# Performance work log

Hardware: AMD Instinct MI355X
Metric: run time of the kernel (lower is better)

The kernel has to match this reference:

```python
import jax, jax.numpy as jnp
import numpy as np

B, N, L, C, H = 8, 300, 4096, 256, 8
DH = C // H  # 32; doubled to 64 after concat with pos/sine embeddings


def _linear_params(key, fan_in, fan_out):
    kw, kb = jax.random.split(key)
    bound = 1.0 / np.sqrt(fan_in)
    W = jax.random.uniform(kw, (fan_out, fan_in), jnp.float32, -bound, bound)
    b = jax.random.uniform(kb, (fan_out,), jnp.float32, -bound, bound)
    return W, b


def setup_inputs() -> dict:
    key = jax.random.key(0)
    ks = jax.random.split(key, 13)
    inp = {
        "query": jax.random.normal(ks[0], (B, N, C), jnp.float32),
        "key": jax.random.normal(ks[1], (B, L, C), jnp.float32),
        "value": jax.random.normal(ks[2], (B, L, C), jnp.float32),
        "query_pos": jax.random.normal(ks[3], (B, N, C), jnp.float32),
        "key_pos": jax.random.normal(ks[4], (B, L, C), jnp.float32),
        "query_sine_embed": jax.random.normal(ks[5], (B, N, C), jnp.float32),
    }
    names = ["qc", "qp", "qs", "kc", "kp", "v", "o"]
    for i, nm in enumerate(names):
        W, b = _linear_params(ks[6 + i], C, C)
        inp[f"W{nm}"] = W
        inp[f"b{nm}"] = b
    return inp


def reference(query, key, value, query_pos, key_pos, query_sine_embed,
              Wqc, bqc, Wqp, bqp, Wqs, bqs, Wkc, bkc, Wkp, bkp, Wv, bv, Wo, bo):
    lin = lambda x, W, b: jnp.einsum("bnc,dc->bnd", x, W) + b
    qc = lin(query, Wqc, bqc)                  # (B, N, C)
    kc = lin(key, Wkc, bkc)                    # (B, L, C)
    v = lin(value, Wv, bv)                     # (B, L, C)
    kp = lin(key_pos, Wkp, bkp)                # (B, L, C)
    qp = lin(query_pos, Wqp, bqp)              # is_first=True branch
    q = qc + qp
    k = kc + kp
    qs = lin(query_sine_embed, Wqs, bqs)
    # split heads and concat content with positional/sine embedding -> head dim 2*DH
    q = jnp.concatenate([q.reshape(B, N, H, DH), qs.reshape(B, N, H, DH)], axis=3)   # (B,N,H,2DH)
    k = jnp.concatenate([k.reshape(B, L, H, DH), kp.reshape(B, L, H, DH)], axis=3)   # (B,L,H,2DH)
    vh = v.reshape(B, L, H, DH)
    scale = (2 * DH) ** -0.5
    attn = jnp.einsum("bnhd,blhd->bhnl", q * scale, k)      # (B,H,N,L)
    attn = jax.nn.softmax(attn, axis=-1)
    out = jnp.einsum("bhnl,blhd->bnhd", attn, vh).reshape(B, N, C)
    out = jnp.einsum("bnc,dc->bnd", out, Wo) + bo
    return query + out  # identity = query
```

## Files before the change

### kernel.cpp

```cpp
#include <hip/hip_runtime.h>
#include <hip/hip_bf16.h>

using bf8_t = __attribute__((ext_vector_type(8))) short;
using bf4_t = __attribute__((ext_vector_type(4))) short;
using u16x4 = __attribute__((ext_vector_type(4))) unsigned short;
using f32x4 = __attribute__((ext_vector_type(4))) float;

constexpr int B_   = 8;
constexpr int N_   = 300;
constexpr int L_   = 4096;
constexpr int C_   = 256;
constexpr int H_   = 8;
constexpr int NPAD = 320;
constexpr int QT_  = 5;
constexpr int SPL_ = 4;
constexpr int TPS_ = 16;
constexpr float SCALE = 0.18033688011112042f;

__device__ __forceinline__ unsigned short f2b(float f) {
  unsigned u = __float_as_uint(f);
  u += 0x7FFFu + ((u >> 16) & 1u);
  return (unsigned short)(u >> 16);
}

__device__ __forceinline__ void stage_cvt16(unsigned short* dst, const float* src) {
#pragma unroll
  for (int half = 0; half < 2; ++half) {
    f32x4 x0 = *(const f32x4*)(src + half * 8);
    f32x4 x1 = *(const f32x4*)(src + half * 8 + 4);
    bf8_t v;
#pragma unroll
    for (int j = 0; j < 4; ++j) { v[j] = (short)f2b(x0[j]); v[4 + j] = (short)f2b(x1[j]); }
    *(bf8_t*)(dst + half * 8) = v;
  }
}

__device__ __forceinline__ void gload_lds16(const void* g, void* l) {
  __builtin_amdgcn_global_load_lds(
      (const __attribute__((address_space(1))) unsigned int*)g,
      (__attribute__((address_space(3))) unsigned int*)l, 16, 0, 0);
}

__device__ __forceinline__ unsigned cvt_pk_bf16(float lo, float hi) {
  unsigned r;
  asm("v_cvt_pk_bf16_f32 %0, %1, %2" : "=v"(r) : "v"(lo), "v"(hi));
  return r;
}

__global__ __launch_bounds__(256) void wcvt_k(
    const float* __restrict__ W0, const float* __restrict__ W1, const float* __restrict__ W2,
    unsigned short* __restrict__ Wq)
{
  const float* W[3] = {W0, W1, W2};
  const int kt = blockIdx.x, i = blockIdx.y;
  const int d = threadIdx.x;
  const float* src = W[i] + (size_t)d * C_ + kt * 64;
  unsigned short* dst = Wq + ((size_t)(i * 4 + kt) * 256 + d) * 64;
#pragma unroll
  for (int g = 0; g < 8; ++g) {
    f32x4 a = *(const f32x4*)(src + g * 8);
    f32x4 b = *(const f32x4*)(src + g * 8 + 4);
    bf8_t v;
#pragma unroll
    for (int j = 0; j < 4; ++j) { v[j] = (short)f2b(a[j]); v[4 + j] = (short)f2b(b[j]); }
    *(bf8_t*)(dst + (g ^ (d & 7)) * 8) = v;
  }
}

__global__ __launch_bounds__(256) void wcvt2_k(
    const float* __restrict__ W0, const float* __restrict__ W1, const float* __restrict__ W2,
    unsigned short* __restrict__ Wk)
{
  const float* W[3] = {W0, W1, W2};
  const int kt = blockIdx.x, i = blockIdx.y;
  const int d = threadIdx.x;
  const float* src = W[i] + (size_t)d * C_ + kt * 32;
  unsigned short* dst = Wk + ((size_t)(i * 8 + kt) * 256 + d) * 32;
#pragma unroll
  for (int g = 0; g < 4; ++g) {
    f32x4 a = *(const f32x4*)(src + g * 8);
    f32x4 b = *(const f32x4*)(src + g * 8 + 4);
    bf8_t v;
#pragma unroll
    for (int j = 0; j < 4; ++j) { v[j] = (short)f2b(a[j]); v[4 + j] = (short)f2b(b[j]); }
    *(bf8_t*)(dst + (g ^ (d & 3)) * 8) = v;
  }
}

__global__ __launch_bounds__(256, 4) void kvproj_k(
    const float* __restrict__ xp, const float* __restrict__ xk, const float* __restrict__ xv,
    const unsigned short* __restrict__ Wk,
    const float* __restrict__ bkp, const float* __restrict__ bkc, const float* __restrict__ bv,
    unsigned short* __restrict__ Kc, unsigned short* __restrict__ Kp, unsigned short* __restrict__ Vt)
{
  __shared__ __align__(16) unsigned short LB[20480];
  const int tid = threadIdx.x, lane = tid & 63, wv = tid >> 6;
  const int fr = lane & 15, fg = lane >> 4;
  const int i = blockIdx.y;
  const int row0 = blockIdx.x * 64;
  const int b = row0 >> 12, ll0 = row0 & (L_ - 1);
  const float* X    = (i == 0) ? xp  : (i == 1) ? xk  : xv;
  const float* bias = (i == 0) ? bkp : (i == 1) ? bkc : bv;

  const int ar = tid >> 2, ac = tid & 3;
  const int agx = (ac ^ (ar & 3)) * 8;

  f32x4 acc[4][4] = {};

  const unsigned short* Wi = Wk + (size_t)i * 8 * 8192;

  auto stageB = [&](int step, int buf) {
    const char* src = (const char*)(Wi + step * 8192);
    char* dst = (char*)(LB + 4096 + buf * 8192);
#pragma unroll
    for (int c = 0; c < 4; ++c) {
      const int off = c * 4096 + tid * 16;
      gload_lds16(src + off, dst + off);
    }
  };
  auto stageA_load = [&](int step, f32x4* arg) {
    const float* s = X + (size_t)(row0 + ar) * C_ + step * 32 + ac * 8;
    arg[0] = *(const f32x4*)s;
    arg[1] = *(const f32x4*)(s + 4);
  };
  auto stageA_write = [&](int buf, const f32x4* arg) {
    bf8_t v;
#pragma unroll
    for (int j = 0; j < 4; ++j) { v[j] = (short)f2b(arg[0][j]); v[4 + j] = (short)f2b(arg[1][j]); }
    *(bf8_t*)(LB + buf * 2048 + ar * 32 + agx) = v;
  };

  {
    f32x4 a0[2];
    stageA_load(0, a0);
    stageB(0, 0);
    stageA_write(0, a0);
  }
  __syncthreads();

  int cur = 0;
  const int gx = (fg ^ (fr & 3)) * 8;
  for (int step = 0; step < 8; ++step) {
    const int nxt = cur ^ 1;
    f32x4 arn[2];
    if (step < 7) {
      stageA_load(step + 1, arn);
      stageB(step + 1, nxt);
    }
    const unsigned short* Ab = LB + cur * 2048;
    const unsigned short* Bb = LB + 4096 + cur * 8192;
    bf8_t xf[4];
#pragma unroll
    for (int mt = 0; mt < 4; ++mt)
      xf[mt] = *(const bf8_t*)(Ab + (mt * 16 + fr) * 32 + gx);
#pragma unroll
    for (int nt = 0; nt < 4; ++nt) {
      bf8_t wf = *(const bf8_t*)(Bb + (wv * 64 + nt * 16 + fr) * 32 + gx);
#pragma unroll
      for (int mt = 0; mt < 4; ++mt)
        acc[nt][mt] = __builtin_amdgcn_mfma_f32_16x16x32_bf16(wf, xf[mt], acc[nt][mt], 0, 0, 0);
    }
    if (step < 7) stageA_write(nxt, arn);
    __syncthreads();
    cur = nxt;
  }

  if (i < 2) {
    unsigned short* outp = (i == 0) ? Kp : Kc;
#pragma unroll
    for (int nt = 0; nt < 4; ++nt) {
      const int d0 = wv * 64 + nt * 16 + fg * 4;
      const f32x4 bb = *(const f32x4*)(bias + d0);
      const int h = d0 >> 5, dh = d0 & 31;
#pragma unroll
      for (int mt = 0; mt < 4; ++mt) {
        const int l = ll0 + mt * 16 + fr;
        u16x4 v;
#pragma unroll
        for (int r = 0; r < 4; ++r) v[r] = f2b(acc[nt][mt][r] + bb[r]);
        *(u16x4*)(outp + ((size_t)(b * H_ + h) * L_ + l) * 32 + dh) = v;
      }
    }
  } else {
    unsigned short* T = LB;
#pragma unroll
    for (int nt = 0; nt < 4; ++nt) {
      const int d0 = wv * 64 + nt * 16 + fg * 4;
      const f32x4 bb = *(const f32x4*)(bias + d0);
#pragma unroll
      for (int mt = 0; mt < 4; ++mt)
#pragma unroll
        for (int r = 0; r < 4; ++r)
          T[(d0 + r) * 68 + mt * 16 + fr] = f2b(acc[nt][mt][r] + bb[r]);
    }
    __syncthreads();
    const int d = tid;
    unsigned short* dst = Vt + ((size_t)(b * H_ + (d >> 5)) * 32 + (d & 31)) * L_ + ll0;
#pragma unroll
    for (int j = 0; j < 16; ++j)
      *(u16x4*)(dst + j * 4) = *(const u16x4*)(T + d * 68 + j * 4);
  }
}

__global__ __launch_bounds__(256, 2) void qproj_k(
    const float* __restrict__ xp, const float* __restrict__ xq, const float* __restrict__ xs,
    const unsigned short* __restrict__ Wq,
    const float* __restrict__ bqp, const float* __restrict__ bqc, const float* __restrict__ bqs,
    unsigned short* __restrict__ Qcat)
{
  __shared__ __align__(16) unsigned short Al[2][64 * 64];
  __shared__ __align__(16) unsigned short Bl[2][256 * 64];
  const int tid = threadIdx.x, lane = tid & 63, wv = tid >> 6;
  const int fr = lane & 15, fg = lane >> 4;
  const int b = blockIdx.x / 5, n0 = (blockIdx.x % 5) * 64;
  const float* Ax[3] = {xp, xq, xs};

  const int sr = tid >> 2, sc = (tid & 3) * 16;
  const int ag = sc >> 3;
  const bool arow_ok = (n0 + sr) < N_;

  f32x4 acc[16] = {};

  auto stageB = [&](int step, int buf) {
    const char* bsrc = (const char*)Wq + (size_t)step * 32768;
    char* bdst = (char*)&Bl[buf][0];
#pragma unroll
    for (int c = 0; c < 8; ++c) {
      const int off = c * 4096 + wv * 1024 + lane * 16;
      gload_lds16(bsrc + off, bdst + off);
    }
  };
  auto stageA_load = [&](int step, f32x4* ar) {
    const int i = step >> 2, kt = step & 3;
    if (arow_ok) {
      const float* src = Ax[i] + ((size_t)b * N_ + n0 + sr) * C_ + kt * 64 + sc;
#pragma unroll
      for (int j = 0; j < 4; ++j) ar[j] = *(const f32x4*)(src + j * 4);
    } else {
#pragma unroll
      for (int j = 0; j < 4; ++j) ar[j] = (f32x4){0.f, 0.f, 0.f, 0.f};
    }
  };
  auto stageA_write = [&](int buf, const f32x4* ar) {
    unsigned short* base = &Al[buf][sr * 64];
    bf8_t v0, v1;
#pragma unroll
    for (int j = 0; j < 4; ++j) {
      v0[j] = (short)f2b(ar[0][j]); v0[4 + j] = (short)f2b(ar[1][j]);
      v1[j] = (short)f2b(ar[2][j]); v1[4 + j] = (short)f2b(ar[3][j]);
    }
    *(bf8_t*)(base + ((ag ^ (sr & 7)) * 8))       = v0;
    *(bf8_t*)(base + (((ag | 1) ^ (sr & 7)) * 8)) = v1;
  };

  {
    f32x4 a0[4];
    stageA_load(0, a0);
    stageB(0, 0);
    stageA_write(0, a0);
  }
  __syncthreads();

  int cur = 0;
  const int xrow = wv * 16 + fr;
  const int n_out = n0 + wv * 16 + fr;
  const bool ok = n_out < N_;
  for (int step = 0; step < 12; ++step) {
    const int nxt = cur ^ 1;
    f32x4 arn[4];
    if (step < 11) {
      stageA_load(step + 1, arn);
      stageB(step + 1, nxt);
    }
    const unsigned short* Ab = &Al[cur][0];
    const unsigned short* Bb = &Bl[cur][0];
#pragma unroll
    for (int kh = 0; kh < 2; ++kh) {
      const int gxx = (4 * kh + fg) ^ (fr & 7);
      bf8_t xf = *(const bf8_t*)(Ab + xrow * 64 + gxx * 8);
#pragma unroll
      for (int nt = 0; nt < 16; ++nt) {
        bf8_t wf = *(const bf8_t*)(Bb + (nt * 16 + fr) * 64 + gxx * 8);
        acc[nt] = __builtin_amdgcn_mfma_f32_16x16x32_bf16(wf, xf, acc[nt], 0, 0, 0);
      }
    }
    if (step == 7 || step == 11) {
      const int off = (step == 7) ? 0 : 32;
#pragma unroll
      for (int nt = 0; nt < 16; ++nt) {
        const int d0 = nt * 16 + fg * 4;
        f32x4 bb = *(const f32x4*)(bqp + d0) + *(const f32x4*)(bqc + d0);
        if (step == 11) bb += *(const f32x4*)(bqs + d0);
        u16x4 v;
#pragma unroll
        for (int r = 0; r < 4; ++r) v[r] = ok ? f2b((acc[nt][r] + bb[r]) * SCALE) : (unsigned short)0;
        *(u16x4*)(Qcat + ((size_t)(b * H_ + (d0 >> 5)) * NPAD + n_out) * 64 + off + (d0 & 31)) = v;
      }
    }
    if (step < 11) stageA_write(nxt, arn);
    __syncthreads();
    cur = nxt;
  }
}

__global__ __launch_bounds__(256, 5) void attn_k(
    const unsigned short* __restrict__ Qcat, const unsigned short* __restrict__ Kc,
    const unsigned short* __restrict__ Kp, const unsigned short* __restrict__ Vt,
    float* __restrict__ PO, float* __restrict__ PM, float* __restrict__ PLs)
{
  __shared__ __align__(16) unsigned short Kcl[2][64 * 32];
  __shared__ __align__(16) unsigned short Kpl[2][64 * 32];
  __shared__ __align__(16) unsigned short Vp[2][32][72];
  const int x = blockIdx.x;
  const int qt = x >> 8;
  const int rem = x & 255;
  const int s = rem & (SPL_ - 1);
  const int h = (rem >> 2) & (H_ - 1);
  const int b = rem >> 5;
  const int n0 = qt * 64;
  const int tid = threadIdx.x, lane = tid & 63, wv = tid >> 6;
  const int fr = lane & 15, fg = lane >> 4;

  const unsigned short* Qb = Qcat + ((size_t)b * H_ + h) * NPAD * 64;
  bf8_t qf[2];
  {
    const int qrow = n0 + wv * 16 + fr;
    qf[0] = *(const bf8_t*)&Qb[(size_t)qrow * 64 + 8 * fg];
    qf[1] = *(const bf8_t*)&Qb[(size_t)qrow * 64 + 32 + 8 * fg];
  }
  float m_r = -1e30f, l_r = 0.f;
  f32x4 o[2] = {};

  const unsigned short* KcB = Kc + ((size_t)b * H_ + h) * L_ * 32;
  const unsigned short* KpB = Kp + ((size_t)b * H_ + h) * L_ * 32;
  const unsigned short* VB  = Vt + ((size_t)b * H_ + h) * 32 * (size_t)L_;

  const int koff = tid * 16;
  const int vd = tid >> 3, vc = (tid & 7) * 8;

  auto stageK = [&](int t, int buf) {
    gload_lds16((const char*)KcB + (size_t)t * 4096 + koff, (char*)&Kcl[buf][0] + koff);
    gload_lds16((const char*)KpB + (size_t)t * 4096 + koff, (char*)&Kpl[buf][0] + koff);
  };

  const int t0 = s * TPS_, t1 = t0 + TPS_;

  stageK(t0, 0);
  bf8_t vreg = *(const bf8_t*)(VB + (size_t)vd * L_ + t0 * 64 + vc);

  int cur = 0;
  for (int t = t0; t < t1; ++t) {
    *(bf8_t*)&Vp[cur][vd][vc] = vreg;
    __syncthreads();
    if (t + 1 < t1) {
      stageK(t + 1, cur ^ 1);
      vreg = *(const bf8_t*)(VB + (size_t)vd * L_ + (t + 1) * 64 + vc);
    }
    f32x4 sc[4] = {};
#pragma unroll
    for (int nf = 0; nf < 4; ++nf) {
      const int kro = (nf * 16 + fr) * 32 + 8 * fg;
      bf8_t kf0 = *(const bf8_t*)&Kcl[cur][kro];
      bf8_t kf1 = *(const bf8_t*)&Kpl[cur][kro];
      sc[nf] = __builtin_amdgcn_mfma_f32_16x16x32_bf16(kf0, qf[0], sc[nf], 0, 0, 0);
      sc[nf] = __builtin_amdgcn_mfma_f32_16x16x32_bf16(kf1, qf[1], sc[nf], 0, 0, 0);
    }
    float mx = fmaxf(fmaxf(sc[0][0], sc[0][1]), fmaxf(sc[0][2], sc[0][3]));
#pragma unroll
    for (int nf = 1; nf < 4; ++nf)
      mx = fmaxf(mx, fmaxf(fmaxf(sc[nf][0], sc[nf][1]), fmaxf(sc[nf][2], sc[nf][3])));
    mx = fmaxf(mx, __shfl_xor(mx, 16));
    mx = fmaxf(mx, __shfl_xor(mx, 32));
    const float mnew = fmaxf(m_r, mx);
    const float corr = exp2f(m_r - mnew);
    float ps = 0.f;
#pragma unroll
    for (int nf = 0; nf < 4; ++nf)
#pragma unroll
      for (int r = 0; r < 4; ++r) {
        const float p = exp2f(sc[nf][r] - mnew);
        sc[nf][r] = p;
        ps += p;
      }
    ps += __shfl_xor(ps, 16);
    ps += __shfl_xor(ps, 32);
    l_r = l_r * corr + ps;
    m_r = mnew;
#pragma unroll
    for (int r = 0; r < 4; ++r) { o[0][r] *= corr; o[1][r] *= corr; }
    unsigned pw[8];
#pragma unroll
    for (int nf = 0; nf < 4; ++nf) {
      pw[2 * nf]     = cvt_pk_bf16(sc[nf][0], sc[nf][1]);
      pw[2 * nf + 1] = cvt_pk_bf16(sc[nf][2], sc[nf][3]);
    }
#pragma unroll
    for (int kh = 0; kh < 2; ++kh) {
      union { unsigned u[4]; bf8_t v; } pu;
      pu.u[0] = pw[4 * kh];     pu.u[1] = pw[4 * kh + 1];
      pu.u[2] = pw[4 * kh + 2]; pu.u[3] = pw[4 * kh + 3];
      const bf8_t pf = pu.v;
#pragma unroll
      for (int df = 0; df < 2; ++df) {
        const unsigned short* vrow = &Vp[cur][df * 16 + fr][0];
        bf4_t va = *(const bf4_t*)(vrow + kh * 32 + fg * 4);
        bf4_t vb = *(const bf4_t*)(vrow + kh * 32 + 16 + fg * 4);
        bf8_t vf;
#pragma unroll
        for (int j = 0; j < 4; ++j) { vf[j] = va[j]; vf[4 + j] = vb[j]; }
        o[df] = __builtin_amdgcn_mfma_f32_16x16x32_bf16(vf, pf, o[df], 0, 0, 0);
      }
    }
    cur ^= 1;
  }
  const int rec = (((b * H_) + h) * QT_ + qt) * SPL_ + s;
  const int q = wv * 16 + fr;
  if (fg == 0) {
    PM [rec * 64 + q] = m_r;
    PLs[rec * 64 + q] = l_r;
  }
#pragma unroll
  for (int df = 0; df < 2; ++df)
    *(f32x4*)(PO + ((size_t)rec * 64 + q) * 32 + df * 16 + fg * 4) = o[df];
}

__global__ __launch_bounds__(256) void combine_k(
    const float* __restrict__ PO, const float* __restrict__ PM, const float* __restrict__ PLs,
    unsigned short* __restrict__ aout)
{
  const int qt = blockIdx.x, h = blockIdx.y, b = blockIdx.z;
  const int tid = threadIdx.x;
  const int row = tid >> 2, dh0 = (tid & 3) * 8;
  const int rec0 = (((b * H_) + h) * QT_ + qt) * SPL_;
  float m[SPL_], w[SPL_];
  float M = -1e30f;
#pragma unroll
  for (int s = 0; s < SPL_; ++s) { m[s] = PM[(rec0 + s) * 64 + row]; M = fmaxf(M, m[s]); }
  float denom = 0.f;
#pragma unroll
  for (int s = 0; s < SPL_; ++s) {
    w[s] = exp2f(m[s] - M);
    denom += w[s] * PLs[(rec0 + s) * 64 + row];
  }
  float num[8] = {};
#pragma unroll
  for (int s = 0; s < SPL_; ++s) {
    const float* po = PO + ((size_t)(rec0 + s) * 64 + row) * 32 + dh0;
    f32x4 a = *(const f32x4*)po;
    f32x4 c = *(const f32x4*)(po + 4);
#pragma unroll
    for (int j = 0; j < 4; ++j) { num[j] += w[s] * a[j]; num[4 + j] += w[s] * c[j]; }
  }
  const int n = qt * 64 + row;
  if (n < N_) {
    const float inv = 1.f / denom;
    bf8_t v;
#pragma unroll
    for (int j = 0; j < 8; ++j) v[j] = (short)f2b(num[j] * inv);
    *(bf8_t*)(aout + ((size_t)b * NPAD + n) * C_ + h * 32 + dh0) = v;
  }
}

__global__ __launch_bounds__(256) void oproj_k(
    const unsigned short* __restrict__ aout, const float* __restrict__ Wo,
    const float* __restrict__ bo, const float* __restrict__ query,
    float* __restrict__ out)
{
  __shared__ __align__(16) unsigned short Al[64][72];
  __shared__ __align__(16) unsigned short Bl[64][72];
  const int b = blockIdx.z, n0 = blockIdx.y * 64, d0 = blockIdx.x * 64;
  const int tid = threadIdx.x, lane = tid & 63, wv = tid >> 6;
  const int wm = wv >> 1, wn = wv & 1;
  const int sr = tid >> 2, sc = (tid & 3) * 16;
  const int fr = lane & 15, fg = lane >> 4;
  f32x4 acc[2][2] = {};

  for (int kt = 0; kt < 4; ++kt) {
    const int k0 = kt * 64;
    {
      const unsigned short* src = aout + ((size_t)b * NPAD + n0 + sr) * C_ + k0 + sc;
      *(bf8_t*)&Al[sr][sc]     = *(const bf8_t*)src;
      *(bf8_t*)&Al[sr][sc + 8] = *(const bf8_t*)(src + 8);
    }
    stage_cvt16(&Bl[sr][sc], Wo + (size_t)(d0 + sr) * C_ + k0 + sc);
    __syncthreads();
#pragma unroll
    for (int kh = 0; kh < 2; ++kh) {
      const int ko = kh * 32 + 8 * fg;
      bf8_t af[2], bq[2];
#pragma unroll
      for (int m = 0; m < 2; ++m) {
        af[m] = *(const bf8_t*)&Al[wm * 32 + m * 16 + fr][ko];
        bq[m] = *(const bf8_t*)&Bl[wn * 32 + m * 16 + fr][ko];
      }
#pragma unroll
      for (int m = 0; m < 2; ++m)
#pragma unroll
        for (int n = 0; n < 2; ++n)
          acc[m][n] = __builtin_amdgcn_mfma_f32_16x16x32_bf16(af[m], bq[n], acc[m][n], 0, 0, 0);
    }
    __syncthreads();
  }
#pragma unroll
  for (int m = 0; m < 2; ++m)
#pragma unroll
    for (int nn = 0; nn < 2; ++nn) {
      const int d = d0 + wn * 32 + nn * 16 + fr;
      const float bb = bo[d];
#pragma unroll
      for (int r = 0; r < 4; ++r) {
        const int n = n0 + wm * 32 + m * 16 + fg * 4 + r;
        if (n < N_) {
          const size_t gi = ((size_t)b * N_ + n) * C_ + d;
          out[gi] = acc[m][nn][r] + bb + query[gi];
        }
      }
    }
}

extern "C" void kernel_launch(void* const* d_in, const int* in_sizes, int n_in,
                              void* d_out, int out_size, void* d_ws, size_t ws_size,
                              hipStream_t stream)
{
  const float* query = (const float*)d_in[0];
  const float* key   = (const float*)d_in[1];
  const float* value = (const float*)d_in[2];
  const float* qpos  = (const float*)d_in[3];
  const float* kpos  = (const float*)d_in[4];
  const float* qsine = (const float*)d_in[5];
  const float* Wqc = (const float*)d_in[6];  const float* bqc = (const float*)d_in[7];
  const float* Wqp = (const float*)d_in[8];  const float* bqp = (const float*)d_in[9];
  const float* Wqs = (const float*)d_in[10]; const float* bqs = (const float*)d_in[11];
  const float* Wkc = (const float*)d_in[12]; const float* bkc = (const float*)d_in[13];
  const float* Wkp = (const float*)d_in[14]; const float* bkp = (const float*)d_in[15];
  const float* Wv  = (const float*)d_in[16]; const float* bv  = (const float*)d_in[17];
  const float* Wo  = (const float*)d_in[18]; const float* bo  = (const float*)d_in[19];

  const size_t qcat_b = (size_t)B_ * H_ * NPAD * 64 * 2;
  const size_t kc_b   = (size_t)B_ * H_ * L_ * 32 * 2;
  const size_t kp_b   = kc_b;
  const size_t vt_b   = kc_b;
  const size_t aout_b = (size_t)B_ * NPAD * C_ * 2;
  const size_t nrec   = (size_t)B_ * H_ * QT_ * SPL_;
  const size_t po_b   = nrec * 64 * 32 * 4;
  const size_t pm_b   = nrec * 64 * 4;
  const size_t pl_b   = nrec * 64 * 4;
  const size_t wsw_b  = (size_t)24 * 256 * 64 * 2;
  if (ws_size < qcat_b + kc_b + kp_b + vt_b + aout_b + po_b + pm_b + pl_b + wsw_b) return;
  char* ws = (char*)d_ws;
  unsigned short* Qcat = (unsigned short*)(ws);
  unsigned short* Kc   = (unsigned short*)(ws + qcat_b);
  unsigned short* Kp   = (unsigned short*)(ws + qcat_b + kc_b);
  unsigned short* Vt   = (unsigned short*)(ws + qcat_b + kc_b + kp_b);
  unsigned short* aout = (unsigned short*)(ws + qcat_b + kc_b + kp_b + vt_b);
  float* PO  = (float*)(ws + qcat_b + kc_b + kp_b + vt_b + aout_b);
  float* PM  = (float*)(ws + qcat_b + kc_b + kp_b + vt_b + aout_b + po_b);
  float* PLs = (float*)(ws + qcat_b + kc_b + kp_b + vt_b + aout_b + po_b + pm_b);
  unsigned short* Wq = (unsigned short*)(ws + qcat_b + kc_b + kp_b + vt_b + aout_b + po_b + pm_b + pl_b);
  unsigned short* Wk = Wq + (size_t)12 * 16384;
  float* out = (float*)d_out;

  wcvt_k   <<<dim3(4, 3),                 256, 0, stream>>>(Wqp, Wqc, Wqs, Wq);
  wcvt2_k  <<<dim3(8, 3),                 256, 0, stream>>>(Wkp, Wkc, Wv, Wk);
  qproj_k  <<<dim3(B_ * QT_),             256, 0, stream>>>(qpos, query, qsine, Wq, bqp, bqc, bqs, Qcat);
  kvproj_k <<<dim3(512, 3),               256, 0, stream>>>(kpos, key, value, Wk, bkp, bkc, bv, Kc, Kp, Vt);
  attn_k   <<<dim3(QT_ * SPL_ * B_ * H_), 256, 0, stream>>>(Qcat, Kc, Kp, Vt, PO, PM, PLs);
  combine_k<<<dim3(QT_, 8, 8),            256, 0, stream>>>(PO, PM, PLs, aout);
  oproj_k  <<<dim3(4, QT_, 8),            256, 0, stream>>>(aout, Wo, bo, query, out);
}
```

Baseline: 131.4 us.

## Drop LDS staging in KV projection and add lazy softmax rescaling

The K/V projection kernel no longer stages inputs or weights through shared memory with barriers. Each wave loads its activation rows and weight fragments straight from global memory into registers, the output columns are split across a new grid z-dimension of 2, and the V transpose uses a per-wave LDS tile with no block-wide sync. Separately, the attention kernel skips the running-max update and the rescaling of o and l unless some lane's new max exceeds the old one by more than 8 (log2 units). This saves exp and multiply work but lets the exponentials reach up to 2^8 before rescaling. The weight conversion kernel also drops the XOR swizzle so the layout matches the direct global reads.

```diff
diff --git a/kernel.cpp b/kernel.cpp
--- a/kernel.cpp
+++ b/kernel.cpp
@@ -83,7 +83,7 @@
     bf8_t v;
 #pragma unroll
     for (int j = 0; j < 4; ++j) { v[j] = (short)f2b(a[j]); v[4 + j] = (short)f2b(b[j]); }
-    *(bf8_t*)(dst + (g ^ (d & 3)) * 8) = v;
+    *(bf8_t*)(dst + g * 8) = v;
   }
 }
 
@@ -93,83 +93,68 @@
     const float* __restrict__ bkp, const float* __restrict__ bkc, const float* __restrict__ bv,
     unsigned short* __restrict__ Kc, unsigned short* __restrict__ Kp, unsigned short* __restrict__ Vt)
 {
-  __shared__ __align__(16) unsigned short LB[20480];
+  __shared__ __align__(16) unsigned short T[4][32 * 68];
   const int tid = threadIdx.x, lane = tid & 63, wv = tid >> 6;
   const int fr = lane & 15, fg = lane >> 4;
-  const int i = blockIdx.y;
+  const int i = blockIdx.y, z = blockIdx.z;
   const int row0 = blockIdx.x * 64;
   const int b = row0 >> 12, ll0 = row0 & (L_ - 1);
   const float* X    = (i == 0) ? xp  : (i == 1) ? xk  : xv;
   const float* bias = (i == 0) ? bkp : (i == 1) ? bkc : bv;
-
-  const int ar = tid >> 2, ac = tid & 3;
-  const int agx = (ac ^ (ar & 3)) * 8;
-
-  f32x4 acc[4][4] = {};
-
-  const unsigned short* Wi = Wk + (size_t)i * 8 * 8192;
-
-  auto stageB = [&](int step, int buf) {
-    const char* src = (const char*)(Wi + step * 8192);
-    char* dst = (char*)(LB + 4096 + buf * 8192);
-#pragma unroll
-    for (int c = 0; c < 4; ++c) {
-      const int off = c * 4096 + tid * 16;
-      gload_lds16(src + off, dst + off);
-    }
+  const int c0 = z * 128 + wv * 32;
+
+  f32x4 acc[2][4] = {};
+  const unsigned short* Wi = Wk + ((size_t)i * 8) * 8192;
+  const float* Xb = X + (size_t)row0 * C_ + fg * 8;
+
+  auto loadA = [&](int t, int mt, f32x4* a) {
+    const float* s = Xb + (size_t)(mt * 16 + fr) * C_ + t * 32;
+    a[0] = *(const f32x4*)s;
+    a[1] = *(const f32x4*)(s + 4);
   };
-  auto stageA_load = [&](int step, f32x4* arg) {
-    const float* s = X + (size_t)(row0 + ar) * C_ + step * 32 + ac * 8;
-    arg[0] = *(const f32x4*)s;
-    arg[1] = *(const f32x4*)(s + 4);
+  auto cvtA = [&](const f32x4* a) {
+    bf8_t v;
+#pragma unroll
+    for (int j = 0; j < 4; ++j) { v[j] = (short)f2b(a[0][j]); v[4 + j] = (short)f2b(a[1][j]); }
+    return v;
   };
-  auto stageA_write = [&](int buf, const f32x4* arg) {
-    bf8_t v;
-#pragma unroll
-    for (int j = 0; j < 4; ++j) { v[j] = (short)f2b(arg[0][j]); v[4 + j] = (short)f2b(arg[1][j]); }
-    *(bf8_t*)(LB + buf * 2048 + ar * 32 + agx) = v;
-  };
-
+
+  bf8_t xf[4];
   {
-    f32x4 a0[2];
-    stageA_load(0, a0);
-    stageB(0, 0);
-    stageA_write(0, a0);
-  }
-  __syncthreads();
-
-  int cur = 0;
-  const int gx = (fg ^ (fr & 3)) * 8;
-  for (int step = 0; step < 8; ++step) {
-    const int nxt = cur ^ 1;
-    f32x4 arn[2];
-    if (step < 7) {
-      stageA_load(step + 1, arn);
-      stageB(step + 1, nxt);
-    }
-    const unsigned short* Ab = LB + cur * 2048;
-    const unsigned short* Bb = LB + 4096 + cur * 8192;
-    bf8_t xf[4];
-#pragma unroll
-    for (int mt = 0; mt < 4; ++mt)
-      xf[mt] = *(const bf8_t*)(Ab + (mt * 16 + fr) * 32 + gx);
-#pragma unroll
-    for (int nt = 0; nt < 4; ++nt) {
-      bf8_t wf = *(const bf8_t*)(Bb + (wv * 64 + nt * 16 + fr) * 32 + gx);
+    f32x4 a0[4][2];
+#pragma unroll
+    for (int mt = 0; mt < 4; ++mt) loadA(0, mt, a0[mt]);
+#pragma unroll
+    for (int mt = 0; mt < 4; ++mt) xf[mt] = cvtA(a0[mt]);
+  }
+
+#pragma unroll
+  for (int t = 0; t < 8; ++t) {
+    f32x4 af[4][2];
+    if (t < 7) {
+#pragma unroll
+      for (int mt = 0; mt < 4; ++mt) loadA(t + 1, mt, af[mt]);
+    }
+    bf8_t wf[2];
+#pragma unroll
+    for (int nt = 0; nt < 2; ++nt)
+      wf[nt] = *(const bf8_t*)(Wi + ((size_t)t * 256 + c0 + nt * 16 + fr) * 32 + fg * 8);
+#pragma unroll
+    for (int nt = 0; nt < 2; ++nt)
 #pragma unroll
       for (int mt = 0; mt < 4; ++mt)
-        acc[nt][mt] = __builtin_amdgcn_mfma_f32_16x16x32_bf16(wf, xf[mt], acc[nt][mt], 0, 0, 0);
-    }
-    if (step < 7) stageA_write(nxt, arn);
-    __syncthreads();
-    cur = nxt;
+        acc[nt][mt] = __builtin_amdgcn_mfma_f32_16x16x32_bf16(wf[nt], xf[mt], acc[nt][mt], 0, 0, 0);
+    if (t < 7) {
+#pragma unroll
+      for (int mt = 0; mt < 4; ++mt) xf[mt] = cvtA(af[mt]);
+    }
   }
 
   if (i < 2) {
     unsigned short* outp = (i == 0) ? Kp : Kc;
 #pragma unroll
-    for (int nt = 0; nt < 4; ++nt) {
-      const int d0 = wv * 64 + nt * 16 + fg * 4;
+    for (int nt = 0; nt < 2; ++nt) {
+      const int d0 = c0 + nt * 16 + fg * 4;
       const f32x4 bb = *(const f32x4*)(bias + d0);
       const int h = d0 >> 5, dh = d0 & 31;
 #pragma unroll
@@ -182,23 +167,25 @@
       }
     }
   } else {
-    unsigned short* T = LB;
-#pragma unroll
-    for (int nt = 0; nt < 4; ++nt) {
-      const int d0 = wv * 64 + nt * 16 + fg * 4;
+    unsigned short* Tw = &T[wv][0];
+#pragma unroll
+    for (int nt = 0; nt < 2; ++nt) {
+      const int d0 = c0 + nt * 16 + fg * 4;
       const f32x4 bb = *(const f32x4*)(bias + d0);
+      const int dl0 = nt * 16 + fg * 4;
 #pragma unroll
       for (int mt = 0; mt < 4; ++mt)
 #pragma unroll
         for (int r = 0; r < 4; ++r)
-          T[(d0 + r) * 68 + mt * 16 + fr] = f2b(acc[nt][mt][r] + bb[r]);
-    }
-    __syncthreads();
-    const int d = tid;
-    unsigned short* dst = Vt + ((size_t)(b * H_ + (d >> 5)) * 32 + (d & 31)) * L_ + ll0;
-#pragma unroll
-    for (int j = 0; j < 16; ++j)
-      *(u16x4*)(dst + j * 4) = *(const u16x4*)(T + d * 68 + j * 4);
+          Tw[(dl0 + r) * 68 + mt * 16 + fr] = f2b(acc[nt][mt][r] + bb[r]);
+    }
+    const int dl = lane >> 1, lh = (lane & 1) * 32;
+    const int d = c0 + dl;
+    unsigned short* dst = Vt + ((size_t)(b * H_ + (d >> 5)) * 32 + (d & 31)) * L_ + ll0 + lh;
+#pragma unroll
+    for (int j = 0; j < 4; ++j)
+      *(u16x4*)(dst + j * 8) = *(const u16x4*)(Tw + dl * 68 + lh + j * 8),
+      *(u16x4*)(dst + j * 8 + 4) = *(const u16x4*)(Tw + dl * 68 + lh + j * 8 + 4);
   }
 }
 
@@ -371,23 +358,26 @@
       mx = fmaxf(mx, fmaxf(fmaxf(sc[nf][0], sc[nf][1]), fmaxf(sc[nf][2], sc[nf][3])));
     mx = fmaxf(mx, __shfl_xor(mx, 16));
     mx = fmaxf(mx, __shfl_xor(mx, 32));
-    const float mnew = fmaxf(m_r, mx);
-    const float corr = exp2f(m_r - mnew);
+    if (!__all(mx <= m_r + 8.f)) {
+      const float mnew = fmaxf(m_r, mx);
+      const float corr = exp2f(m_r - mnew);
+      l_r *= corr;
+#pragma unroll
+      for (int r = 0; r < 4; ++r) { o[0][r] *= corr; o[1][r] *= corr; }
+      m_r = mnew;
+    }
     float ps = 0.f;
 #pragma unroll
     for (int nf = 0; nf < 4; ++nf)
 #pragma unroll
       for (int r = 0; r < 4; ++r) {
-        const float p = exp2f(sc[nf][r] - mnew);
+        const float p = exp2f(sc[nf][r] - m_r);
         sc[nf][r] = p;
         ps += p;
       }
     ps += __shfl_xor(ps, 16);
     ps += __shfl_xor(ps, 32);
-    l_r = l_r * corr + ps;
-    m_r = mnew;
-#pragma unroll
-    for (int r = 0; r < 4; ++r) { o[0][r] *= corr; o[1][r] *= corr; }
+    l_r += ps;
     unsigned pw[8];
 #pragma unroll
     for (int nf = 0; nf < 4; ++nf) {
@@ -563,7 +553,7 @@
   wcvt_k   <<<dim3(4, 3),                 256, 0, stream>>>(Wqp, Wqc, Wqs, Wq);
   wcvt2_k  <<<dim3(8, 3),                 256, 0, stream>>>(Wkp, Wkc, Wv, Wk);
   qproj_k  <<<dim3(B_ * QT_),             256, 0, stream>>>(qpos, query, qsine, Wq, bqp, bqc, bqs, Qcat);
-  kvproj_k <<<dim3(512, 3),               256, 0, stream>>>(kpos, key, value, Wk, bkp, bkc, bv, Kc, Kp, Vt);
+  kvproj_k <<<dim3(512, 3, 2),            256, 0, stream>>>(kpos, key, value, Wk, bkp, bkc, bv, Kc, Kp, Vt);
   attn_k   <<<dim3(QT_ * SPL_ * B_ * H_), 256, 0, stream>>>(Qcat, Kc, Kp, Vt, PO, PM, PLs);
   combine_k<<<dim3(QT_, 8, 8),            256, 0, stream>>>(PO, PM, PLs, aout);
   oproj_k  <<<dim3(4, QT_, 8),            256, 0, stream>>>(aout, Wo, bo, query, out);
```

Result: slower. 202.2 us (+53.9%).
